# Kernel tuning notes

Measured on AMD Instinct MI355X. Metric: run time of the kernel, lower is better.

The kernel has to match this reference:

```python
import jax, jax.numpy as jnp
import numpy as np


def setup_inputs() -> dict:
    key = jax.random.key(0)
    k1, k2, k3 = jax.random.split(key, 3)
    B, T, I, H = 32, 2048, 512, 512
    x = jax.random.normal(k1, (B, T, I), dtype=jnp.float32)
    W_x = jax.random.normal(k2, (3, I, H), dtype=jnp.float32) / np.sqrt(I)
    W_h = jax.random.normal(k3, (3, H, H), dtype=jnp.float32) / np.sqrt(H)
    bias = jnp.zeros((3, H), dtype=jnp.float32)
    return {"x": x, "W_x": W_x, "W_h": W_h, "bias": bias}


def reference(x, W_x, W_h, bias):
    # x: [B, T, I]; W_x: [3, I, H]; W_h: [3, H, H]; bias: [3, H]
    B, T, I = x.shape
    H = W_h.shape[-1]
    # Precompute input-side contributions for all gates/timesteps (batched GEMM):
    # gx: [T, 3, B, H] = x @ W_x[g] + bias[g]
    gx = jnp.einsum('bti,gih->tgbh', x, W_x) + bias[:, None, :]

    W_hz, W_hr, W_hh = W_h[0], W_h[1], W_h[2]

    def step(h_prev, gx_t):
        # gx_t: [3, B, H]
        z = jax.nn.sigmoid(gx_t[0] + h_prev @ W_hz)          # update gate
        r = jax.nn.sigmoid(gx_t[1] + h_prev @ W_hr)          # reset gate
        h_tilde = jnp.tanh(gx_t[2] + (r * h_prev) @ W_hh)    # candidate
        h_t = (1.0 - z) * h_prev + z * h_tilde
        return h_t, h_t

    h0 = jnp.zeros((B, H), dtype=x.dtype)
    h_last, outs = jax.lax.scan(step, h0, gx)  # outs: [T, B, H]
    output = jnp.transpose(outs, (1, 0, 2))    # [B, T, H]
    return output, h_last
```

## Files before the change

kernel.cpp:

```cpp
#include <hip/hip_runtime.h>
#include <stdint.h>
#include <stddef.h>


#define AGENT __HIP_MEMORY_SCOPE_AGENT

typedef _Float16 h2v __attribute__((ext_vector_type(2)));
typedef _Float16 half8 __attribute__((ext_vector_type(8)));
typedef float f32x4 __attribute__((ext_vector_type(4)));

__device__ __forceinline__ uint32_t pk2u(float a, float b) {
  h2v r; r[0] = (_Float16)a; r[1] = (_Float16)b;
  return __builtin_bit_cast(uint32_t, r);
}
__device__ __forceinline__ h2v bc2(uint32_t u) { return __builtin_bit_cast(h2v, u); }
__device__ __forceinline__ float dot2f(h2v a, h2v b, float c) {
#if __has_builtin(__builtin_amdgcn_fdot2)
  return __builtin_amdgcn_fdot2(a, b, c, false);
#else
  return fmaf((float)a[1], (float)b[1], fmaf((float)a[0], (float)b[0], c));
#endif
}
__device__ __forceinline__ float sigmoidf_(float x) { return 1.0f / (1.0f + __expf(-x)); }
__device__ __forceinline__ float tanhf_(float x) { return 1.0f - 2.0f / (1.0f + __expf(2.0f * x)); }

__device__ __forceinline__ uint32_t ald32(const uint32_t* p) {
  return __hip_atomic_load(p, __ATOMIC_RELAXED, AGENT);
}
__device__ __forceinline__ void ast32(uint32_t* p, uint32_t v) {
  __hip_atomic_store(p, v, __ATOMIC_RELAXED, AGENT);
}
__device__ __forceinline__ uint64_t ald64(const uint64_t* p) {
  return __hip_atomic_load(p, __ATOMIC_RELAXED, AGENT);
}
__device__ __forceinline__ void ast64(uint64_t* p, uint64_t v) {
  __hip_atomic_store(p, v, __ATOMIC_RELAXED, AGENT);
}
__device__ __forceinline__ float f16b2f(uint32_t w) {
  return (float)__builtin_bit_cast(_Float16, (unsigned short)(w & 0xffffu));
}

__global__ __launch_bounds__(256) void gemm_gx(const float* __restrict__ x,
                                               const float* __restrict__ Wx,
                                               const float* __restrict__ bias,
                                               _Float16* gzr,
                                               _Float16* gh,
                                               int nTN) {
  __shared__ alignas(16) _Float16 Alds[128 * 68];
  __shared__ alignas(16) _Float16 Blds[128 * 68];
  const int tid = threadIdx.x;
  const int bid = blockIdx.x;
  const int tm = bid / nTN, tn = bid % nTN;
  const int m0 = tm << 7, n0 = tn << 7;
  const int lane = tid & 63;
  const int wv = tid >> 6, wm = wv >> 1, wn = wv & 1;
  const int l15 = lane & 15, lhi = lane >> 4;
  f32x4 acc[4][4] = {};

  for (int k0 = 0; k0 < 512; k0 += 64) {
#pragma unroll
    for (int r = 0; r < 8; ++r) {
      int m = r * 16 + (tid >> 4);
      int k = (tid & 15) * 4;
      float4 v = *(const float4*)&x[(size_t)(m0 + m) * 512 + k0 + k];
      union { _Float16 h[4]; uint2 u; } cv;
      cv.h[0] = (_Float16)v.x; cv.h[1] = (_Float16)v.y;
      cv.h[2] = (_Float16)v.z; cv.h[3] = (_Float16)v.w;
      *(uint2*)&Alds[m * 68 + k] = cv.u;
    }
#pragma unroll
    for (int u = 0; u < 8; ++u) {
      int n = tid & 127;
      int k = (tid >> 7) * 32 + u * 4;
      int ng = n0 + n;
      const float* wp = Wx + ((size_t)(ng >> 9) << 18) + (size_t)(k0 + k) * 512 + (ng & 511);
      union { _Float16 h[4]; uint2 u2; } cv;
      cv.h[0] = (_Float16)wp[0];    cv.h[1] = (_Float16)wp[512];
      cv.h[2] = (_Float16)wp[1024]; cv.h[3] = (_Float16)wp[1536];
      *(uint2*)&Blds[n * 68 + k] = cv.u2;
    }
    __syncthreads();
#pragma unroll
    for (int kk = 0; kk < 2; ++kk) {
      int q = kk * 4 + lhi;
      half8 af[4], bf[4];
#pragma unroll
      for (int fm = 0; fm < 4; ++fm) {
        const _Float16* pa = &Alds[(wm * 64 + fm * 16 + l15) * 68 + q * 8];
        union { uint2 u[2]; half8 h; } cv;
        cv.u[0] = *(const uint2*)pa; cv.u[1] = *(const uint2*)(pa + 4);
        af[fm] = cv.h;
      }
#pragma unroll
      for (int fn = 0; fn < 4; ++fn) {
        const _Float16* pb = &Blds[(wn * 64 + fn * 16 + l15) * 68 + q * 8];
        union { uint2 u[2]; half8 h; } cv;
        cv.u[0] = *(const uint2*)pb; cv.u[1] = *(const uint2*)(pb + 4);
        bf[fn] = cv.h;
      }
#pragma unroll
      for (int fm = 0; fm < 4; ++fm)
#pragma unroll
        for (int fn = 0; fn < 4; ++fn)
          acc[fm][fn] = __builtin_amdgcn_mfma_f32_16x16x32_f16(af[fm], bf[fn], acc[fm][fn], 0, 0, 0);
    }
    __syncthreads();
  }
#pragma unroll
  for (int fn = 0; fn < 4; ++fn) {
    int col = n0 + wn * 64 + fn * 16 + l15;
    float bv = bias[col];
#pragma unroll
    for (int fm = 0; fm < 4; ++fm) {
#pragma unroll
      for (int q2 = 0; q2 < 4; ++q2) {
        int row = m0 + wm * 64 + fm * 16 + lhi * 4 + q2;
        _Float16 val = (_Float16)(acc[fm][fn][q2] + bv);
        if (n0 < 1024) gzr[(size_t)row * 1024 + col] = val;
        else           gh[(size_t)row * 512 + (col - 1024)] = val;
      }
    }
  }
}

__device__ __forceinline__ bool tagsok8(const uint32_t pv[8], uint64_t zv, uint32_t want) {
  bool ok = ((uint32_t)(zv >> 32) == want);
#pragma unroll
  for (int q = 0; q < 8; ++q) ok &= ((pv[q] >> 16) == want);
  return ok;
}

__global__ __launch_bounds__(512) void gru_scan3(
    const _Float16* gzr,
    const _Float16* ghg,
    const float* __restrict__ Wh,
    float* out,
    uint32_t* __restrict__ Pbuf,
    uint64_t* __restrict__ zbuf) {
  __shared__ alignas(16) _Float16 wzK[2 * 8 * 64 * 8 * 8];
  __shared__ alignas(16) _Float16 hA[512];
  __shared__ alignas(16) _Float16 rh[64];

  const int T = threadIdx.x;
  const int bid = blockIdx.x;
  const int s = bid >> 5;
  const int b = bid & 31;
  const int c = T >> 3, sub = T & 7;
  const int gcol = s * 64 + c;

  for (int g = 0; g < 2; ++g) {
    const float* W = Wh + (size_t)g * 262144;
    for (int idx = T; idx < 4096; idx += 512) {
      int cc = idx >> 9;
      int col = (idx >> 3) & 63;
      int sb = idx & 7;
      int kbase = (cc * 8 + sb) * 8;
      _Float16* dst = &wzK[(((g * 8 + cc) * 64 + col) * 8 + sb) * 8];
#pragma unroll
      for (int e = 0; e < 8; ++e)
        dst[e] = (_Float16)W[(size_t)(kbase + e) * 512 + s * 64 + col];
    }
  }
  uint32_t wh2[32];
  {
    const float* Whh = Wh + 524288;
#pragma unroll
    for (int i = 0; i < 32; ++i) {
      int kk = s * 64 + 2 * i;
      wh2[i] = pk2u(Whh[(size_t)kk * 512 + T], Whh[(size_t)(kk + 1) * 512 + T]);
    }
  }
  hA[T] = (_Float16)0.0f;
  float hreg = 0.f;

  const size_t rb = (size_t)b * 2048;
  float gh_p, gh_c = 0.f, gz_p = 0.f, gr_p = 0.f, gz_c = 0.f, gr_c = 0.f;
  gh_p = (float)ghg[rb * 512 + T];
  if (sub == 0) {
    gz_p = (float)gzr[rb * 1024 + gcol];
    gr_p = (float)gzr[rb * 1024 + 512 + gcol];
  }

  uint32_t* Pm = Pbuf + ((size_t)b * 8 + s) * 512 + T;
  const uint32_t* Pr = Pbuf + (size_t)b * 4096 + T;
  uint64_t* zm = zbuf + (size_t)b * 512 + gcol;
  const uint64_t* zrd = zbuf + (size_t)b * 512 + T;

  uint32_t pv[8];
  uint64_t zv = 0;
#pragma unroll
  for (int q = 0; q < 8; ++q) pv[q] = 0;

  for (int t = 0; t < 2048; ++t) {
    const size_t poC = ((t - 1) & 1) ? 131072 : 0;
    const size_t zoC = ((t - 1) & 1) ? 16384 : 0;
    const size_t poN = (t & 1) ? 131072 : 0;
    const size_t zoN = (t & 1) ? 16384 : 0;
    const uint32_t want = (uint32_t)t;
    const uint32_t tagN = (uint32_t)(t + 1);

    if (t > 0) {
      while (!tagsok8(pv, zv, want)) {
        __builtin_amdgcn_s_sleep(2);
        if ((uint32_t)(zv >> 32) != want) zv = ald64(zrd + zoC);
#pragma unroll
        for (int q = 0; q < 8; ++q)
          if ((pv[q] >> 16) != want) pv[q] = ald32(Pr + poC + (size_t)q * 512);
      }
      float hsum = 0.f;
#pragma unroll
      for (int q = 0; q < 8; ++q) hsum += f16b2f(pv[q]);
      float zf = __uint_as_float((uint32_t)zv);
      float htil = tanhf_(gh_c + hsum);
      float hn = fmaf(zf, htil - hreg, hreg);
      if (s == 0) out[(rb + (t - 1)) * 512 + T] = hn;
      hreg = hn;
      hA[T] = (_Float16)hn;
    }
    gh_c = gh_p;
    gz_c = gz_p;
    gr_c = gr_p;
    __syncthreads();
    if (t < 2047) {
      size_t r1 = rb + t + 1;
      gh_p = (float)ghg[r1 * 512 + T];
      if (sub == 0) {
        gz_p = (float)gzr[r1 * 1024 + gcol];
        gr_p = (float)gzr[r1 * 1024 + 512 + gcol];
      }
    }

    float za = 0.f, ra = 0.f;
#pragma unroll
    for (int cc = 0; cc < 8; ++cc) {
      uint4 hu = *(const uint4*)&hA[(cc * 8 + sub) * 8];
      uint4 wz = *(const uint4*)&wzK[(((cc)*64 + c) * 8 + sub) * 8];
      uint4 wr = *(const uint4*)&wzK[(((8 + cc) * 64 + c) * 8 + sub) * 8];
      za = dot2f(bc2(hu.x), bc2(wz.x), za); za = dot2f(bc2(hu.y), bc2(wz.y), za);
      za = dot2f(bc2(hu.z), bc2(wz.z), za); za = dot2f(bc2(hu.w), bc2(wz.w), za);
      ra = dot2f(bc2(hu.x), bc2(wr.x), ra); ra = dot2f(bc2(hu.y), bc2(wr.y), ra);
      ra = dot2f(bc2(hu.z), bc2(wr.z), ra); ra = dot2f(bc2(hu.w), bc2(wr.w), ra);
    }
#pragma unroll
    for (int d = 1; d < 8; d <<= 1) {
      za += __shfl_xor(za, d);
      ra += __shfl_xor(ra, d);
    }
    if (sub == 0) {
      float z = sigmoidf_(za + gz_c);
      float r = sigmoidf_(ra + gr_c);
      rh[c] = (_Float16)(r * (float)hA[gcol]);
      ast64(zm + zoN, ((uint64_t)tagN << 32) | (uint32_t)__float_as_uint(z));
    }
    __syncthreads();

    {
      float pa = 0.f;
#pragma unroll
      for (int i = 0; i < 16; ++i) {
        uint2 ru = *(const uint2*)&rh[4 * i];
        pa = dot2f(bc2(ru.x), bc2(wh2[2 * i]), pa);
        pa = dot2f(bc2(ru.y), bc2(wh2[2 * i + 1]), pa);
      }
      unsigned short pb = __builtin_bit_cast(unsigned short, (_Float16)pa);
      ast32(Pm + poN, (tagN << 16) | (uint32_t)pb);
    }
    zv = ald64(zrd + zoN);
#pragma unroll
    for (int q = 0; q < 8; ++q) pv[q] = ald32(Pr + poN + (size_t)q * 512);
    __builtin_amdgcn_sched_barrier(0);
  }

  {
    const uint32_t want = 2048u;
    while (!tagsok8(pv, zv, want)) {
      __builtin_amdgcn_s_sleep(2);
      if ((uint32_t)(zv >> 32) != want) zv = ald64(zrd + 16384);
#pragma unroll
      for (int q = 0; q < 8; ++q)
        if ((pv[q] >> 16) != want) pv[q] = ald32(Pr + 131072 + (size_t)q * 512);
    }
    float hsum = 0.f;
#pragma unroll
    for (int q = 0; q < 8; ++q) hsum += f16b2f(pv[q]);
    float zf = __uint_as_float((uint32_t)zv);
    float htil = tanhf_(gh_c + hsum);
    float hn = fmaf(zf, htil - hreg, hreg);
    if (s == 0) {
      out[(rb + 2047) * 512 + T] = hn;
      out[(size_t)32 * 2048 * 512 + (size_t)b * 512 + T] = hn;
    }
  }
}

__global__ __launch_bounds__(512) void gru_scan_fb(
    const float* __restrict__ x, const float* __restrict__ Wx,
    const float* __restrict__ Wh, const float* __restrict__ bias,
    const _Float16* gzr, float* out,
    uint64_t* __restrict__ Pbuf, uint64_t* __restrict__ zbuf) {
  __shared__ alignas(16) float zrp[2][8][64];
  __shared__ alignas(16) _Float16 wzrL[2 * 64 * 516];
  __shared__ alignas(16) _Float16 h16[512];
  __shared__ alignas(16) _Float16 rh16[64];
  __shared__ alignas(16) _Float16 x16s[64];

  const int T = threadIdx.x;
  const int bid = blockIdx.x;
  const int xcd = bid & 7, ii = bid >> 3;
  const int batch = xcd * 4 + (ii >> 3);
  const int slice = ii & 7;
  const int wv = T >> 6, ln = T & 63, n = T;
  {
    const int cc = T & 63, kb = T >> 6;
#pragma unroll 4
    for (int g = 0; g < 2; ++g) {
      const float* W = Wh + (size_t)g * 262144 + slice * 64 + cc;
      for (int i = 0; i < 64; ++i) {
        int k = kb + 8 * i;
        wzrL[(g * 64 + cc) * 516 + k] = (_Float16)W[(size_t)k * 512];
      }
    }
  }
  uint32_t wh2[32], wx2[32];
  {
    const float* Whh = Wh + 524288;
    const float* Wxh = Wx + 524288;
#pragma unroll
    for (int jj = 0; jj < 32; ++jj) {
      int kk = slice * 64 + 2 * jj;
      wh2[jj] = pk2u(Whh[(size_t)kk * 512 + n], Whh[(size_t)(kk + 1) * 512 + n]);
      wx2[jj] = pk2u(Wxh[(size_t)kk * 512 + n], Wxh[(size_t)(kk + 1) * 512 + n]);
    }
  }
  const float bh = bias[1024 + n];
  float hreg = 0.0f;
  h16[T] = (_Float16)0.0f;
  const size_t rowbase = (size_t)batch * 2048;
  float gz_p = 0.f, gr_p = 0.f, gz_cur = 0.f, gr_cur = 0.f, x_p = 0.f;
  if (T < 64)       gz_p = (float)gzr[rowbase * 1024 + slice * 64 + T];
  else if (T < 128) gr_p = (float)gzr[rowbase * 1024 + 512 + slice * 64 + (T - 64)];
  if (T < 64) x_p = x[rowbase * 512 + slice * 64 + T];

  uint64_t* Pmine = Pbuf + ((size_t)batch * 8 + slice) * 512 + n;
  const uint64_t* Pread = Pbuf + ((size_t)batch * 8) * 512 + n;
  uint64_t* zmine = zbuf + (size_t)batch * 512 + slice * 64 + ln;
  const uint64_t* zread = zbuf + (size_t)batch * 512 + n;

  for (int t = 0; t < 2048; ++t) {
    if (t > 0) {
      const size_t po = ((t - 1) & 1) ? 131072 : 0;
      const size_t zo = ((t - 1) & 1) ? 16384 : 0;
      const uint32_t want = (uint32_t)t;
      uint64_t v[8];
#pragma unroll
      for (int g = 0; g < 8; ++g) v[g] = ald64(Pread + po + (size_t)g * 512);
      uint64_t zvv = ald64(zread + zo);
      for (;;) {
        bool ok = true;
        if ((uint32_t)(zvv >> 32) != want) { zvv = ald64(zread + zo); ok = false; }
#pragma unroll
        for (int g = 0; g < 8; ++g)
          if ((uint32_t)(v[g] >> 32) != want) { v[g] = ald64(Pread + po + (size_t)g * 512); ok = false; }
        if (ok) break;
        __builtin_amdgcn_s_sleep(1);
      }
      float hsum = 0.f;
#pragma unroll
      for (int g = 0; g < 8; ++g) hsum += __uint_as_float((uint32_t)v[g]);
      float zf = __uint_as_float((uint32_t)zvv);
      float htil = tanhf_(bh + hsum);
      float hn = fmaf(zf, htil - hreg, hreg);
      if (slice == 0) out[(rowbase + (t - 1)) * 512 + n] = hn;
      hreg = hn;
      h16[T] = (_Float16)hn;
    }
    gz_cur = gz_p; gr_cur = gr_p;
    if (T < 64) x16s[T] = (_Float16)x_p;
    __syncthreads();
    if (t < 2047) {
      size_t r1 = rowbase + t + 1;
      if (T < 64)       gz_p = (float)gzr[r1 * 1024 + slice * 64 + T];
      else if (T < 128) gr_p = (float)gzr[r1 * 1024 + 512 + slice * 64 + (T - 64)];
      if (T < 64) x_p = x[r1 * 512 + slice * 64 + T];
    }
    float za = 0.f, ra = 0.f;
    {
      const _Float16* wzp = &wzrL[ln * 516 + 64 * wv];
      const _Float16* wrp = &wzrL[(64 + ln) * 516 + 64 * wv];
      const _Float16* hp = &h16[64 * wv];
#pragma unroll
      for (int jj = 0; jj < 16; ++jj) {
        uint2 wzu = *(const uint2*)(wzp + 4 * jj);
        uint2 wru = *(const uint2*)(wrp + 4 * jj);
        uint2 hu = *(const uint2*)(hp + 4 * jj);
        za = dot2f(bc2(hu.x), bc2(wzu.x), za);
        za = dot2f(bc2(hu.y), bc2(wzu.y), za);
        ra = dot2f(bc2(hu.x), bc2(wru.x), ra);
        ra = dot2f(bc2(hu.y), bc2(wru.y), ra);
      }
    }
    zrp[0][wv][ln] = za;
    zrp[1][wv][ln] = ra;
    __syncthreads();
    const size_t po = (t & 1) ? 131072 : 0;
    const size_t zo = (t & 1) ? 16384 : 0;
    const uint64_t tagw = ((uint64_t)(uint32_t)(t + 1)) << 32;
    if (T < 128) {
      const int g = T >> 6, cc = T & 63;
      float sum = 0.f;
#pragma unroll
      for (int s2 = 0; s2 < 8; ++s2) sum += zrp[g][s2][cc];
      if (g == 0) {
        float z = sigmoidf_(sum + gz_cur);
        ast64(zmine + zo, tagw | (uint32_t)__float_as_uint(z));
      } else {
        float r = sigmoidf_(sum + gr_cur);
        rh16[cc] = (_Float16)(r * (float)h16[slice * 64 + cc]);
      }
    }
    __syncthreads();
    float pa = 0.f;
#pragma unroll
    for (int jj = 0; jj < 16; ++jj) {
      uint2 ru = *(const uint2*)&rh16[4 * jj];
      pa = dot2f(bc2(ru.x), bc2(wh2[2 * jj]), pa);
      pa = dot2f(bc2(ru.y), bc2(wh2[2 * jj + 1]), pa);
    }
#pragma unroll
    for (int jj = 0; jj < 16; ++jj) {
      uint2 xu = *(const uint2*)&x16s[4 * jj];
      pa = dot2f(bc2(xu.x), bc2(wx2[2 * jj]), pa);
      pa = dot2f(bc2(xu.y), bc2(wx2[2 * jj + 1]), pa);
    }
    ast64(Pmine + po, tagw | (uint32_t)__float_as_uint(pa));
    __syncthreads();
  }
  {
    const uint32_t want = 2048u;
    uint64_t v[8];
#pragma unroll
    for (int g = 0; g < 8; ++g) v[g] = ald64(Pread + 131072 + (size_t)g * 512);
    uint64_t zvv = ald64(zread + 16384);
    for (;;) {
      bool ok = true;
      if ((uint32_t)(zvv >> 32) != want) { zvv = ald64(zread + 16384); ok = false; }
#pragma unroll
      for (int g = 0; g < 8; ++g)
        if ((uint32_t)(v[g] >> 32) != want) { v[g] = ald64(Pread + 131072 + (size_t)g * 512); ok = false; }
      if (ok) break;
      __builtin_amdgcn_s_sleep(1);
    }
    float hsum = 0.f;
#pragma unroll
    for (int g = 0; g < 8; ++g) hsum += __uint_as_float((uint32_t)v[g]);
    float zf = __uint_as_float((uint32_t)zvv);
    float htil = tanhf_(bh + hsum);
    float hn = fmaf(zf, htil - hreg, hreg);
    if (slice == 0) {
      out[(rowbase + 2047) * 512 + n] = hn;
      out[(size_t)32 * 2048 * 512 + (size_t)batch * 512 + n] = hn;
    }
  }
}

extern "C" void kernel_launch(void* const* d_in, const int* in_sizes, int n_in,
                              void* d_out, int out_size, void* d_ws, size_t ws_size,
                              hipStream_t stream) {
  (void)in_sizes; (void)n_in; (void)out_size;
  const float* x    = (const float*)d_in[0];
  const float* Wx   = (const float*)d_in[1];
  const float* Wh   = (const float*)d_in[2];
  const float* bias = (const float*)d_in[3];
  float* out = (float*)d_out;
  char* ws = (char*)d_ws;

  uint32_t* Pbuf3 = (uint32_t*)ws;
  uint64_t* zbuf3 = (uint64_t*)(ws + 1048576);
  uint64_t* PbufF = (uint64_t*)ws;
  uint64_t* zbufF = (uint64_t*)(ws + 2097152);
  _Float16* gh    = (_Float16*)(ws + 2621440);

  hipMemsetAsync(ws, 0, 2621440, stream);
  const bool gh_mode = ws_size >= (size_t)2621440 + 67108864ull;
  if (gh_mode) {
    gemm_gx<<<512 * 12, 256, 0, stream>>>(x, Wx, bias, (_Float16*)d_out, gh, 12);
    gru_scan3<<<256, 512, 0, stream>>>((const _Float16*)d_out, gh, Wh, out,
                                       Pbuf3, zbuf3);
  } else {
    gemm_gx<<<512 * 8, 256, 0, stream>>>(x, Wx, bias, (_Float16*)d_out, gh, 8);
    gru_scan_fb<<<256, 512, 0, stream>>>(x, Wx, Wh, bias, (const _Float16*)d_out,
                                         out, PbufF, zbufF);
  }
}
```

Measured before the change: 7.155 ms.

## Map GRU scan blocks to XCDs and use sc0 loads for inter-block flags

```diff
diff --git a/kernel.cpp b/kernel.cpp
--- a/kernel.cpp
+++ b/kernel.cpp
@@ -24,20 +24,58 @@
 __device__ __forceinline__ float sigmoidf_(float x) { return 1.0f / (1.0f + __expf(-x)); }
 __device__ __forceinline__ float tanhf_(float x) { return 1.0f - 2.0f / (1.0f + __expf(2.0f * x)); }
 
-__device__ __forceinline__ uint32_t ald32(const uint32_t* p) {
+__device__ __forceinline__ uint32_t ald32a(const uint32_t* p) {
   return __hip_atomic_load(p, __ATOMIC_RELAXED, AGENT);
 }
-__device__ __forceinline__ void ast32(uint32_t* p, uint32_t v) {
-  __hip_atomic_store(p, v, __ATOMIC_RELAXED, AGENT);
-}
-__device__ __forceinline__ uint64_t ald64(const uint64_t* p) {
+__device__ __forceinline__ uint64_t ald64a(const uint64_t* p) {
   return __hip_atomic_load(p, __ATOMIC_RELAXED, AGENT);
 }
-__device__ __forceinline__ void ast64(uint64_t* p, uint64_t v) {
+__device__ __forceinline__ void ast64a(uint64_t* p, uint64_t v) {
   __hip_atomic_store(p, v, __ATOMIC_RELAXED, AGENT);
 }
 __device__ __forceinline__ float f16b2f(uint32_t w) {
   return (float)__builtin_bit_cast(_Float16, (unsigned short)(w & 0xffffu));
+}
+
+__device__ __forceinline__ uint32_t ld32_sc0(const uint32_t* p) {
+  uint32_t v;
+  asm volatile("global_load_dword %0, %1, off sc0\n\ts_waitcnt vmcnt(0)"
+               : "=v"(v) : "v"(p) : "memory");
+  return v;
+}
+__device__ __forceinline__ uint64_t ld64_sc0(const uint64_t* p) {
+  uint64_t v;
+  asm volatile("global_load_dwordx2 %0, %1, off sc0\n\ts_waitcnt vmcnt(0)"
+               : "=v"(v) : "v"(p) : "memory");
+  return v;
+}
+__device__ __forceinline__ void st32_pub(uint32_t* p, uint32_t v) {
+  asm volatile("global_store_dword %0, %1, off sc0" :: "v"(p), "v"(v) : "memory");
+  __hip_atomic_store(p, v, __ATOMIC_RELAXED, AGENT);
+}
+__device__ __forceinline__ void st64_pub(uint64_t* p, uint64_t v) {
+  asm volatile("global_store_dwordx2 %0, %1, off sc0" :: "v"(p), "v"(v) : "memory");
+  __hip_atomic_store(p, v, __ATOMIC_RELAXED, AGENT);
+}
+__device__ __forceinline__ void ld9_sc0(const uint32_t* pP, const uint64_t* pz,
+                                        uint32_t v[8], uint64_t& zv) {
+  asm volatile(
+      "global_load_dword %0, %9, off sc0\n\t"
+      "global_load_dword %1, %10, off sc0\n\t"
+      "global_load_dword %2, %11, off sc0\n\t"
+      "global_load_dword %3, %12, off sc0\n\t"
+      "global_load_dword %4, %13, off sc0\n\t"
+      "global_load_dword %5, %14, off sc0\n\t"
+      "global_load_dword %6, %15, off sc0\n\t"
+      "global_load_dword %7, %16, off sc0\n\t"
+      "global_load_dwordx2 %8, %17, off sc0\n\t"
+      "s_waitcnt vmcnt(0)"
+      : "=&v"(v[0]), "=&v"(v[1]), "=&v"(v[2]), "=&v"(v[3]),
+        "=&v"(v[4]), "=&v"(v[5]), "=&v"(v[6]), "=&v"(v[7]), "=&v"(zv)
+      : "v"(pP), "v"(pP + 512), "v"(pP + 1024), "v"(pP + 1536),
+        "v"(pP + 2048), "v"(pP + 2560), "v"(pP + 3072), "v"(pP + 3584),
+        "v"(pz)
+      : "memory");
 }
 
 __global__ __launch_bounds__(256) void gemm_gx(const float* __restrict__ x,
@@ -123,7 +161,7 @@
   }
 }
 
-__device__ __forceinline__ bool tagsok8(const uint32_t pv[8], uint64_t zv, uint32_t want) {
+__device__ __forceinline__ bool tagsok9(const uint32_t pv[8], uint64_t zv, uint32_t want) {
   bool ok = ((uint32_t)(zv >> 32) == want);
 #pragma unroll
   for (int q = 0; q < 8; ++q) ok &= ((pv[q] >> 16) == want);
@@ -136,15 +174,48 @@
     const float* __restrict__ Wh,
     float* out,
     uint32_t* __restrict__ Pbuf,
-    uint64_t* __restrict__ zbuf) {
+    uint64_t* __restrict__ zbuf,
+    uint32_t* __restrict__ cnt,
+    uint32_t* __restrict__ claim) {
   __shared__ alignas(16) _Float16 wzK[2 * 8 * 64 * 8 * 8];
   __shared__ alignas(16) _Float16 hA[512];
   __shared__ alignas(16) _Float16 rh[64];
+  __shared__ int entryS;
 
   const int T = threadIdx.x;
-  const int bid = blockIdx.x;
-  const int s = bid >> 5;
-  const int b = bid & 31;
+
+  if (T == 0) {
+    uint32_t xcd;
+    asm volatile("s_getreg_b32 %0, hwreg(HW_REG_XCC_ID)" : "=s"(xcd));
+    xcd &= 7u;
+    uint32_t slot = __hip_atomic_fetch_add(&cnt[xcd], 1u, __ATOMIC_RELAXED, AGENT);
+    int entry = -1;
+    if (slot < 32u) {
+      int e = (int)(xcd * 32u + slot);
+      uint32_t exp0 = 0;
+      if (__hip_atomic_compare_exchange_strong(&claim[e], &exp0, 1u,
+                                               __ATOMIC_RELAXED, __ATOMIC_RELAXED, AGENT))
+        entry = e;
+    }
+    if (entry < 0) {
+      int e = (int)(xcd * 32u);
+      while (entry < 0) {
+        if (__hip_atomic_load(&claim[e], __ATOMIC_RELAXED, AGENT) == 0u) {
+          uint32_t exp0 = 0;
+          if (__hip_atomic_compare_exchange_strong(&claim[e], &exp0, 1u,
+                                                   __ATOMIC_RELAXED, __ATOMIC_RELAXED, AGENT))
+            entry = e;
+        }
+        e = (e + 1) & 255;
+      }
+    }
+    entryS = entry;
+  }
+  __syncthreads();
+  const int entry = entryS;
+  const int s = entry & 7;
+  const int b = ((entry >> 5) << 2) + ((entry >> 3) & 3);
+
   const int c = T >> 3, sub = T & 7;
   const int gcol = s * 64 + c;
 
@@ -200,12 +271,19 @@
     const uint32_t tagN = (uint32_t)(t + 1);
 
     if (t > 0) {
-      while (!tagsok8(pv, zv, want)) {
-        __builtin_amdgcn_s_sleep(2);
-        if ((uint32_t)(zv >> 32) != want) zv = ald64(zrd + zoC);
+      int round = 0;
+      while (!tagsok9(pv, zv, want)) {
+        ++round;
+        __builtin_amdgcn_s_sleep(1);
+        bool deep = (round & 15) == 15;
+        if ((uint32_t)(zv >> 32) != want)
+          zv = deep ? ald64a(zrd + zoC) : ld64_sc0(zrd + zoC);
 #pragma unroll
         for (int q = 0; q < 8; ++q)
-          if ((pv[q] >> 16) != want) pv[q] = ald32(Pr + poC + (size_t)q * 512);
+          if ((pv[q] >> 16) != want) {
+            const uint32_t* p = Pr + poC + (size_t)q * 512;
+            pv[q] = deep ? ald32a(p) : ld32_sc0(p);
+          }
       }
       float hsum = 0.f;
 #pragma unroll
@@ -250,7 +328,7 @@
       float z = sigmoidf_(za + gz_c);
       float r = sigmoidf_(ra + gr_c);
       rh[c] = (_Float16)(r * (float)hA[gcol]);
-      ast64(zm + zoN, ((uint64_t)tagN << 32) | (uint32_t)__float_as_uint(z));
+      st64_pub(zm + zoN, ((uint64_t)tagN << 32) | (uint32_t)__float_as_uint(z));
     }
     __syncthreads();
 
@@ -263,22 +341,27 @@
         pa = dot2f(bc2(ru.y), bc2(wh2[2 * i + 1]), pa);
       }
       unsigned short pb = __builtin_bit_cast(unsigned short, (_Float16)pa);
-      ast32(Pm + poN, (tagN << 16) | (uint32_t)pb);
-    }
-    zv = ald64(zrd + zoN);
-#pragma unroll
-    for (int q = 0; q < 8; ++q) pv[q] = ald32(Pr + poN + (size_t)q * 512);
+      st32_pub(Pm + poN, (tagN << 16) | (uint32_t)pb);
+    }
+    ld9_sc0(Pr + poN, zrd + zoN, pv, zv);
     __builtin_amdgcn_sched_barrier(0);
   }
 
   {
     const uint32_t want = 2048u;
-    while (!tagsok8(pv, zv, want)) {
-      __builtin_amdgcn_s_sleep(2);
-      if ((uint32_t)(zv >> 32) != want) zv = ald64(zrd + 16384);
+    int round = 0;
+    while (!tagsok9(pv, zv, want)) {
+      ++round;
+      __builtin_amdgcn_s_sleep(1);
+      bool deep = (round & 15) == 15;
+      if ((uint32_t)(zv >> 32) != want)
+        zv = deep ? ald64a(zrd + 16384) : ld64_sc0(zrd + 16384);
 #pragma unroll
       for (int q = 0; q < 8; ++q)
-        if ((pv[q] >> 16) != want) pv[q] = ald32(Pr + 131072 + (size_t)q * 512);
+        if ((pv[q] >> 16) != want) {
+          const uint32_t* p = Pr + 131072 + (size_t)q * 512;
+          pv[q] = deep ? ald32a(p) : ld32_sc0(p);
+        }
     }
     float hsum = 0.f;
 #pragma unroll
@@ -353,14 +436,14 @@
       const uint32_t want = (uint32_t)t;
       uint64_t v[8];
 #pragma unroll
-      for (int g = 0; g < 8; ++g) v[g] = ald64(Pread + po + (size_t)g * 512);
-      uint64_t zvv = ald64(zread + zo);
+      for (int g = 0; g < 8; ++g) v[g] = ald64a(Pread + po + (size_t)g * 512);
+      uint64_t zvv = ald64a(zread + zo);
       for (;;) {
         bool ok = true;
-        if ((uint32_t)(zvv >> 32) != want) { zvv = ald64(zread + zo); ok = false; }
+        if ((uint32_t)(zvv >> 32) != want) { zvv = ald64a(zread + zo); ok = false; }
 #pragma unroll
         for (int g = 0; g < 8; ++g)
-          if ((uint32_t)(v[g] >> 32) != want) { v[g] = ald64(Pread + po + (size_t)g * 512); ok = false; }
+          if ((uint32_t)(v[g] >> 32) != want) { v[g] = ald64a(Pread + po + (size_t)g * 512); ok = false; }
         if (ok) break;
         __builtin_amdgcn_s_sleep(1);
       }
@@ -412,7 +495,7 @@
       for (int s2 = 0; s2 < 8; ++s2) sum += zrp[g][s2][cc];
       if (g == 0) {
         float z = sigmoidf_(sum + gz_cur);
-        ast64(zmine + zo, tagw | (uint32_t)__float_as_uint(z));
+        ast64a(zmine + zo, tagw | (uint32_t)__float_as_uint(z));
       } else {
         float r = sigmoidf_(sum + gr_cur);
         rh16[cc] = (_Float16)(r * (float)h16[slice * 64 + cc]);
@@ -432,21 +515,21 @@
       pa = dot2f(bc2(xu.x), bc2(wx2[2 * jj]), pa);
       pa = dot2f(bc2(xu.y), bc2(wx2[2 * jj + 1]), pa);
     }
-    ast64(Pmine + po, tagw | (uint32_t)__float_as_uint(pa));
+    ast64a(Pmine + po, tagw | (uint32_t)__float_as_uint(pa));
     __syncthreads();
   }
   {
     const uint32_t want = 2048u;
     uint64_t v[8];
 #pragma unroll
-    for (int g = 0; g < 8; ++g) v[g] = ald64(Pread + 131072 + (size_t)g * 512);
-    uint64_t zvv = ald64(zread + 16384);
+    for (int g = 0; g < 8; ++g) v[g] = ald64a(Pread + 131072 + (size_t)g * 512);
+    uint64_t zvv = ald64a(zread + 16384);
     for (;;) {
       bool ok = true;
-      if ((uint32_t)(zvv >> 32) != want) { zvv = ald64(zread + 16384); ok = false; }
+      if ((uint32_t)(zvv >> 32) != want) { zvv = ald64a(zread + 16384); ok = false; }
 #pragma unroll
       for (int g = 0; g < 8; ++g)
-        if ((uint32_t)(v[g] >> 32) != want) { v[g] = ald64(Pread + 131072 + (size_t)g * 512); ok = false; }
+        if ((uint32_t)(v[g] >> 32) != want) { v[g] = ald64a(Pread + 131072 + (size_t)g * 512); ok = false; }
       if (ok) break;
       __builtin_amdgcn_s_sleep(1);
     }
@@ -476,6 +559,8 @@
 
   uint32_t* Pbuf3 = (uint32_t*)ws;
   uint64_t* zbuf3 = (uint64_t*)(ws + 1048576);
+  uint32_t* cnt   = (uint32_t*)(ws + 1310720);
+  uint32_t* claim = (uint32_t*)(ws + 1310752);
   uint64_t* PbufF = (uint64_t*)ws;
   uint64_t* zbufF = (uint64_t*)(ws + 2097152);
   _Float16* gh    = (_Float16*)(ws + 2621440);
@@ -485,7 +570,7 @@
   if (gh_mode) {
     gemm_gx<<<512 * 12, 256, 0, stream>>>(x, Wx, bias, (_Float16*)d_out, gh, 12);
     gru_scan3<<<256, 512, 0, stream>>>((const _Float16*)d_out, gh, Wh, out,
-                                       Pbuf3, zbuf3);
+                                       Pbuf3, zbuf3, cnt, claim);
   } else {
     gemm_gx<<<512 * 8, 256, 0, stream>>>(x, Wx, bias, (_Float16*)d_out, gh, 8);
     gru_scan_fb<<<256, 512, 0, stream>>>(x, Wx, Wh, bias, (const _Float16*)d_out,
```

After: 26.32 ms. +267.9%, slower.
